# Kernel optimization log

Measured on AMD Instinct MI355X. Metric: run time of the kernel, lower is better.

## Reference

```python
import jax, jax.numpy as jnp
import numpy as np

R, N, C, E, H, NC = 25, 256, 64, 128, 8, 27


def _layernorm(x, w, b, axes, eps):
    m = x.mean(axis=axes, keepdims=True)
    v = x.var(axis=axes, keepdims=True)
    return (x - m) / jnp.sqrt(v + eps) * w + b


def _mha(emb_ln, idx, WQ, WK):
    # emb_ln: (R*N, E); idx: (L,) district indices
    ew = emb_ln.reshape(R, N, E)[idx]                       # (L,N,E) gather of district blocks
    Q = jnp.einsum('lne,hfe->lhnf', ew, WQ)                 # torch Linear: x @ W.T
    K = jnp.einsum('lne,hfe->lhnf', ew, WK)
    QK = jnp.einsum('lhnf,lhmf->lhnm', Q, K) / jnp.sqrt(jnp.float32(E))
    return jax.nn.softmax(QK, axis=2)                       # torch softmax(dim=1) over (L,n,n)


def setup_inputs() -> dict:
    key = jax.random.key(0)
    ks = jax.random.split(key, 16)
    inp = {
        'business_structure_target': jax.random.normal(ks[0], (R, C, N, 4), jnp.float32),
        'business_structure_infected': jax.random.normal(ks[1], (R, C, N, 4), jnp.float32),
        'customer_structure_target': jax.random.normal(ks[2], (R, C, N, NC, 4), jnp.float32),
        'customer_structure_infected': jax.random.normal(ks[3], (R, C, N, NC, 4), jnp.float32),
        'index_target_idx': jax.random.randint(ks[4], (R, C), 0, R),
        'index_infected_idx': jax.random.randint(ks[5], (R, C), 0, R),
        'covid_outbreak_business': jax.random.randint(ks[6], (R, C), 0, N),
        'emb_table': jax.random.normal(ks[7], (R * N, E), jnp.float32),
        'ln_emb_w': jnp.ones((E,), jnp.float32),
        'ln_emb_b': jnp.zeros((E,), jnp.float32),
        'WQ_trg': jax.random.normal(ks[8], (H, E, E), jnp.float32) * 0.05,
        'WK_trg': jax.random.normal(ks[9], (H, E, E), jnp.float32) * 0.05,
        'WQ_inf': jax.random.normal(ks[10], (H, E, E), jnp.float32) * 0.05,
        'WK_inf': jax.random.normal(ks[11], (H, E, E), jnp.float32) * 0.05,
        'W_os': jax.random.normal(ks[12], (E, E), jnp.float32) * 0.05,
        'b_os': jnp.zeros((E,), jnp.float32),
        'bs_w': jnp.ones((C, N), jnp.float32), 'bs_b': jnp.zeros((C, N), jnp.float32),
        'cs_w': jnp.ones((C, N), jnp.float32), 'cs_b': jnp.zeros((C, N), jnp.float32),
        'os_w': jnp.ones((C, N), jnp.float32), 'os_b': jnp.zeros((C, N), jnp.float32),
    }
    return inp


def reference(business_structure_target, business_structure_infected,
              customer_structure_target, customer_structure_infected,
              index_target_idx, index_infected_idx, covid_outbreak_business,
              emb_table, ln_emb_w, ln_emb_b,
              WQ_trg, WK_trg, WQ_inf, WK_inf,
              W_os, b_os, bs_w, bs_b, cs_w, cs_b, os_w, os_b):
    # mean over feature dim, then slicing per original forward
    bst = business_structure_target.mean(-1)[:R, 0]        # (R,N)
    bsi = business_structure_infected.mean(-1)[0]          # (C,N)
    cst = customer_structure_target.mean(-1)[:R, 0]        # (R,N,NC)
    csi = customer_structure_infected.mean(-1)[0]          # (C,N,NC)

    emb_ln = _layernorm(emb_table, ln_emb_w, ln_emb_b, -1, 1e-16)
    idx_t = index_target_idx[:R, 0]                        # (R,)
    idx_i = index_infected_idx[0]                          # (C,)

    attn_t = _mha(emb_ln, idx_t, WQ_trg, WK_trg)           # (R,H,N,N)
    BR_t = jnp.einsum('ln,lhnm->lmh', bst, attn_t)         # (R,N,H)
    attn_i = _mha(emb_ln, idx_i, WQ_inf, WK_inf)           # (C,H,N,N)
    BR_i = jnp.einsum('cn,chnm->cmh', bsi, attn_i)         # (C,N,H)

    # cosine similarity over head dim, broadcast (R,1,N,H) x (1,C,N,H)
    a = BR_t[:, None]
    b = BR_i[None]
    dot = jnp.sum(a * b, -1)
    na = jnp.linalg.norm(a, axis=-1)
    nb = jnp.linalg.norm(b, axis=-1)
    BS = dot / jnp.maximum(na * nb, 1e-15)                 # (R,C,N)

    # Jensen-Shannon-style KLD over consumer dim (log_target=True semantics)
    log_p = jax.nn.log_softmax(cst, -1)[:, None]           # (R,1,N,NC)
    log_q = jax.nn.log_softmax(csi, -1)[None]              # (1,C,N,NC)
    log_m = jax.nn.log_softmax((log_p + log_q) / 2, -1)
    kl_p = (jnp.exp(log_m) * (log_m - log_p)).mean(-1)
    kl_q = (jnp.exp(log_m) * (log_m - log_q)).mean(-1)
    CS = -(kl_p + kl_q) / 2                                # (R,C,N)

    biz = covid_outbreak_business[0]                       # (C,)
    inf_emb = emb_table[idx_i * N + biz]                   # (C,E) raw (non-LN) embedding
    proj = inf_emb @ W_os.T + b_os
    OS = (proj @ emb_table.T).reshape(C, R, N).transpose(1, 0, 2)  # (R,C,N)

    BS = _layernorm(BS, bs_w, bs_b, (-2, -1), 1e-5)
    CS = _layernorm(CS, cs_w, cs_b, (-2, -1), 1e-5)
    OS = _layernorm(OS, os_w, os_b, (-2, -1), 1e-5)
    return BS, CS, OS
```

## Files before the change

kernel.cpp:

```cpp
#include <hip/hip_runtime.h>
#include <math.h>

#define R_ 25
#define N_ 256
#define C_ 64
#define E_ 128
#define H_ 8
#define NC_ 27
#define SQS 28

typedef _Float16 f16x8 __attribute__((ext_vector_type(8)));
typedef float f32x16 __attribute__((ext_vector_type(16)));

union HU { ushort s; _Float16 h; };
__device__ __forceinline__ ushort ftoh(float f) { HU u; u.h = (_Float16)f; return u.s; }
__device__ __forceinline__ float htof(ushort s) { HU u; u.s = s; return (float)u.h; }

__device__ __forceinline__ float waveReduceSum(float v) {
  #pragma unroll
  for (int off = 32; off > 0; off >>= 1) v += __shfl_xor(v, off);
  return v;
}

__global__ __launch_bounds__(256) void k_prep(
    const float* __restrict__ emb, const float* __restrict__ ln_w,
    const float* __restrict__ ln_b, ushort* __restrict__ emb16,
    const float* __restrict__ bus_t, const float* __restrict__ bus_i,
    float* __restrict__ bst, float* __restrict__ bsi,
    const float* __restrict__ cus_t, const float* __restrict__ cus_i,
    float* __restrict__ Ssq, float* __restrict__ Tsq,
    const int* __restrict__ idx_t, const int* __restrict__ idx_i,
    int* __restrict__ cnt, int* __restrict__ lst,
    const int* __restrict__ biz, const float* __restrict__ Wos,
    const float* __restrict__ bos, float* __restrict__ projb) {
  __shared__ float er2[2][E_];
  int bid = blockIdx.x, t = threadIdx.x;
  if (bid < 1600) {
    int row = bid * 4 + (t >> 6);
    int lane = t & 63;
    const float2* x = (const float2*)(emb + (size_t)row * E_);
    float2 v = x[lane];
    float s = waveReduceSum(v.x + v.y);
    float m = s * (1.0f / 128.0f);
    float d0 = v.x - m, d1 = v.y - m;
    float ss = waveReduceSum(d0 * d0 + d1 * d1);
    float inv = 1.0f / sqrtf(ss * (1.0f / 128.0f) + 1e-16f);
    float2 wv = ((const float2*)ln_w)[lane];
    float2 bv = ((const float2*)ln_b)[lane];
    uint u = (uint)ftoh(d0 * inv * wv.x + bv.x) | ((uint)ftoh(d1 * inv * wv.y + bv.y) << 16);
    ((uint*)emb16)[(size_t)row * 64 + lane] = u;
  } else if (bid < 1689) {
    int i = (bid - 1600) * 256 + t;
    if (i < R_ * N_) {
      size_t row = (size_t)(i >> 8) * (C_ * N_) + (i & 255);
      float4 v = *(const float4*)&bus_t[row * 4];
      bst[i] = (v.x + v.y + v.z + v.w) * 0.25f;
    }
    int j = i - R_ * N_;
    if (j >= 0 && j < C_ * N_) {
      float4 v = *(const float4*)&bus_i[(size_t)j * 4];
      bsi[j] = (v.x + v.y + v.z + v.w) * 0.25f;
    }
  } else if (bid < 1778) {
    int i = (bid - 1689) * 256 + t;
    const float* src; float* dst; size_t base; int oi;
    if (i < R_ * N_) {
      src = cus_t; dst = Ssq; oi = i;
      base = ((size_t)(i >> 8) * (C_ * N_) + (i & 255)) * (NC_ * 4);
    } else {
      int j = i - R_ * N_;
      if (j >= C_ * N_) return;
      src = cus_i; dst = Tsq; oi = j;
      base = ((size_t)(j >> 8) * N_ + (j & 255)) * (NC_ * 4);
    }
    float v[NC_];
    float mx = -1e30f;
    #pragma unroll
    for (int j = 0; j < NC_; ++j) {
      float4 q = *(const float4*)&src[base + j * 4];
      v[j] = (q.x + q.y + q.z + q.w) * 0.25f;
      mx = fmaxf(mx, v[j]);
    }
    float se = 0.0f;
    #pragma unroll
    for (int j = 0; j < NC_; ++j) se += expf(v[j] - mx);
    float lse = mx + logf(se);
    #pragma unroll
    for (int j = 0; j < NC_; ++j) dst[(size_t)oi * SQS + j] = expf(0.5f * (v[j] - lse));
    dst[(size_t)oi * SQS + NC_] = 0.0f;
  } else if (bid == 1778) {
    if (t < 2 * R_) cnt[t] = 0;
    __syncthreads();
    if (t < R_) {
      int rr = idx_t[t * C_];
      int pos = atomicAdd(&cnt[rr], 1);
      lst[rr * 64 + pos] = t;
    }
    if (t < C_) {
      int rr = idx_i[t];
      int pos = atomicAdd(&cnt[R_ + rr], 1);
      lst[(R_ + rr) * 64 + pos] = t;
    }
  } else {
    int pb = bid - 1779;
    int ci = t >> 7, f = t & 127;
    int c = pb * 2 + ci;
    int row = idx_i[c] * N_ + biz[c];
    er2[ci][f] = emb[(size_t)row * E_ + f];
    __syncthreads();
    float acc = bos[f];
    const float* wr = &Wos[(size_t)f * E_];
    const float* er = er2[ci];
    for (int e = 0; e < E_; e += 4) {
      float4 w4 = *(const float4*)&wr[e];
      acc += er[e] * w4.x + er[e + 1] * w4.y + er[e + 2] * w4.z + er[e + 3] * w4.w;
    }
    projb[c * E_ + f] = acc;
  }
}

__global__ __launch_bounds__(512) void k_gt_mfma(
    const float* __restrict__ WQt_, const float* __restrict__ WKt_,
    const float* __restrict__ WQi_, const float* __restrict__ WKi_,
    ushort* __restrict__ Gt) {
  int h = blockIdx.x, set = blockIdx.y;
  const float* WQ = (set ? WQi_ : WQt_) + ((size_t)h << 14);
  const float* WK = (set ? WKi_ : WKt_) + ((size_t)h << 14);
  __shared__ uint QT[128 * 64];
  __shared__ uint KT[128 * 64];
  int t = threadIdx.x;
  for (int j = t; j < 8192; j += 512) {
    int e = j & 127, f2 = j >> 7;
    int wi = (f2 << 8) + e;
    float q0 = WQ[wi], q1 = WQ[wi + 128];
    float k0 = WK[wi], k1 = WK[wi + 128];
    int idx = (e << 6) + (f2 ^ ((e & 15) << 2));
    QT[idx] = (uint)ftoh(q0) | ((uint)ftoh(q1) << 16);
    KT[idx] = (uint)ftoh(k0) | ((uint)ftoh(k1) << 16);
  }
  __syncthreads();
  int w = t >> 6, l = t & 63, lo = l & 31, hi = l >> 5;
  int m0 = (w & 3) << 5, n0 = (w >> 2) << 6;
  f32x16 acc[2];
  #pragma unroll
  for (int i = 0; i < 2; ++i)
    #pragma unroll
    for (int j = 0; j < 16; ++j) acc[i][j] = 0.0f;
  int mrow = m0 + lo;
  #pragma unroll
  for (int ks = 0; ks < 8; ++ks) {
    int f2b = (ks << 3) + (hi << 2);
    f16x8 a = *(const f16x8*)&KT[(mrow << 6) + (f2b ^ ((mrow & 15) << 2))];
    #pragma unroll
    for (int tl = 0; tl < 2; ++tl) {
      int ncol = n0 + (tl << 5) + lo;
      f16x8 b = *(const f16x8*)&QT[(ncol << 6) + (f2b ^ ((ncol & 15) << 2))];
      acc[tl] = __builtin_amdgcn_mfma_f32_32x32x16_f16(a, b, acc[tl], 0, 0, 0);
    }
  }
  const float scale = 0.08838834764831845f;
  ushort* Go = Gt + (((size_t)(set * H_ + h)) << 14);
  #pragma unroll
  for (int tl = 0; tl < 2; ++tl)
    #pragma unroll
    for (int rg = 0; rg < 16; ++rg) {
      int row = m0 + (rg & 3) + ((rg >> 2) << 3) + (hi << 2);
      int col = n0 + (tl << 5) + lo;
      Go[(row << 7) + col] = ftoh(acc[tl][rg] * scale);
    }
}

__global__ __launch_bounds__(512) void k_attn_fused(
    const ushort* __restrict__ emb16, const ushort* __restrict__ GtAll,
    const int* __restrict__ cnt, const int* __restrict__ lst,
    const float* __restrict__ bst, const float* __restrict__ bsi,
    float* __restrict__ BRt, float* __restrict__ BRi) {
  int r = blockIdx.x, h = blockIdx.y, set = blockIdx.z;
  int g = set * R_ + r;
  int L = cnt[g];
  if (L == 0) return;
  __shared__ ushort ELN[256 * 128];
  __shared__ ushort TA[128 * 128];
  __shared__ ushort TB[128 * 128];
  __shared__ float redA[8 * 128];
  __shared__ float redB[8 * 128];
  __shared__ float gM[128], gD[128];
  int t = threadIdx.x;
  const uint4* Ep = (const uint4*)(emb16 + ((size_t)r << 15));
  for (int c = t; c < 4096; c += 512) {
    int n = c >> 4, s = c & 15;
    uint4 v = Ep[c];
    *(uint4*)&ELN[(n << 7) + ((s << 3) ^ ((n & 15) << 3))] = v;
  }
  const uint4* Gp = (const uint4*)(GtAll + ((size_t)(set * H_ + h) << 14));
  for (int c = t; c < 2048; c += 512) {
    int e2 = c >> 4, s = c & 15;
    uint4 v = Gp[c];
    *(uint4*)&TA[(e2 << 7) + ((s << 3) ^ ((e2 & 15) << 3))] = v;
  }
  __syncthreads();
  int w = t >> 6, l = t & 63, lo = l & 31, hi = l >> 5;
  f32x16 tacc[4];
  #pragma unroll
  for (int i = 0; i < 4; ++i)
    #pragma unroll
    for (int j = 0; j < 16; ++j) tacc[i][j] = 0.0f;
  int n = (w << 5) + lo;
  #pragma unroll
  for (int ks = 0; ks < 8; ++ks) {
    f16x8 a = *(const f16x8*)&ELN[(n << 7) + (((ks << 4) + (hi << 3)) ^ ((n & 15) << 3))];
    #pragma unroll
    for (int tl = 0; tl < 4; ++tl) {
      int f = (tl << 5) + lo;
      f16x8 b = *(const f16x8*)&TA[(f << 7) + (((ks << 4) + (hi << 3)) ^ ((f & 15) << 3))];
      tacc[tl] = __builtin_amdgcn_mfma_f32_32x32x16_f16(a, b, tacc[tl], 0, 0, 0);
    }
  }
  __syncthreads();
  {
    ushort* Tl = (w < 4) ? TA : TB;
    #pragma unroll
    for (int tl = 0; tl < 4; ++tl)
      #pragma unroll
      for (int rg = 0; rg < 16; ++rg) {
        int row = ((w & 3) << 5) + (rg & 3) + ((rg >> 2) << 3) + (hi << 2);
        int col = (tl << 5) + lo;
        Tl[(row << 7) + (col ^ ((row & 15) << 3))] = ftoh(tacc[tl][rg]);
      }
  }
  __syncthreads();
  const float* wv = set ? bsi : bst;
  float* BR = set ? BRi : BRt;
  const ushort* Tl = (w < 4) ? TA : TB;
  int rrow = n & 127;
  int baseRow = (w << 5) + (hi << 2);
  for (int mh = 0; mh < 2; ++mh) {
    f32x16 acc[4];
    #pragma unroll
    for (int i = 0; i < 4; ++i)
      #pragma unroll
      for (int j = 0; j < 16; ++j) acc[i][j] = 0.0f;
    #pragma unroll
    for (int ks = 0; ks < 8; ++ks) {
      f16x8 a = *(const f16x8*)&Tl[(rrow << 7) + (((ks << 4) + (hi << 3)) ^ ((rrow & 15) << 3))];
      #pragma unroll
      for (int tl = 0; tl < 4; ++tl) {
        int m = (mh << 7) + (tl << 5) + lo;
        f16x8 b = *(const f16x8*)&ELN[(m << 7) + (((ks << 4) + (hi << 3)) ^ ((m & 15) << 3))];
        acc[tl] = __builtin_amdgcn_mfma_f32_32x32x16_f16(a, b, acc[tl], 0, 0, 0);
      }
    }
    #pragma unroll
    for (int tl = 0; tl < 4; ++tl) {
      float mx = acc[tl][0];
      #pragma unroll
      for (int rg = 1; rg < 16; ++rg) mx = fmaxf(mx, acc[tl][rg]);
      mx = fmaxf(mx, __shfl_xor(mx, 32));
      if (hi == 0) redA[(w << 7) + (tl << 5) + lo] = mx;
    }
    __syncthreads();
    if (t < 128) {
      float gm = redA[t];
      #pragma unroll
      for (int ww = 1; ww < 8; ++ww) gm = fmaxf(gm, redA[(ww << 7) + t]);
      gM[t] = gm;
    }
    __syncthreads();
    #pragma unroll
    for (int tl = 0; tl < 4; ++tl) {
      float gmv = gM[(tl << 5) + lo];
      float s = 0.0f;
      #pragma unroll
      for (int rg = 0; rg < 16; ++rg) {
        acc[tl][rg] = __expf(acc[tl][rg] - gmv);
        s += acc[tl][rg];
      }
      s += __shfl_xor(s, 32);
      if (hi == 0) redB[(w << 7) + (tl << 5) + lo] = s;
    }
    __syncthreads();
    if (t < 128) {
      float d = 0.0f;
      #pragma unroll
      for (int ww = 0; ww < 8; ++ww) d += redB[(ww << 7) + t];
      gD[t] = d;
    }
    __syncthreads();
    for (int li = 0; li < L; ++li) {
      int ll = lst[g * 64 + li];
      float wreg[16];
      #pragma unroll
      for (int rg = 0; rg < 16; ++rg)
        wreg[rg] = wv[ll * N_ + baseRow + (rg & 3) + ((rg >> 2) << 3)];
      #pragma unroll
      for (int tl = 0; tl < 4; ++tl) {
        float part = 0.0f;
        #pragma unroll
        for (int rg = 0; rg < 16; ++rg) part += wreg[rg] * acc[tl][rg];
        part += __shfl_xor(part, 32);
        if (hi == 0) redA[(w << 7) + (tl << 5) + lo] = part;
      }
      __syncthreads();
      if (t < 128) {
        float s = 0.0f;
        #pragma unroll
        for (int ww = 0; ww < 8; ++ww) s += redA[(ww << 7) + t];
        BR[((size_t)ll * N_ + (mh << 7) + t) * H_ + h] = s / gD[t];
      }
      __syncthreads();
    }
  }
}

__global__ __launch_bounds__(256) void k_bscs_os(
    const float* __restrict__ BRt, const float* __restrict__ BRi,
    const float* __restrict__ Ssq, const float* __restrict__ Tsq,
    const float* __restrict__ emb, const float* __restrict__ projb,
    float* __restrict__ outBS, float* __restrict__ outCS,
    float* __restrict__ outOS) {
  __shared__ float pr[8][E_];
  int bid = blockIdx.x, t = threadIdx.x;
  if (bid < 1600) {
    int i = bid * 256 + t;
    int n = i & 255, c = (i >> 8) & 63, l = i >> 14;
    const float4* a = (const float4*)&BRt[((size_t)l * N_ + n) * H_];
    const float4* b = (const float4*)&BRi[((size_t)c * N_ + n) * H_];
    float4 a0 = a[0], a1 = a[1], b0 = b[0], b1 = b[1];
    float dot = a0.x * b0.x + a0.y * b0.y + a0.z * b0.z + a0.w * b0.w
              + a1.x * b1.x + a1.y * b1.y + a1.z * b1.z + a1.w * b1.w;
    float na = a0.x * a0.x + a0.y * a0.y + a0.z * a0.z + a0.w * a0.w
             + a1.x * a1.x + a1.y * a1.y + a1.z * a1.z + a1.w * a1.w;
    float nb = b0.x * b0.x + b0.y * b0.y + b0.z * b0.z + b0.w * b0.w
             + b1.x * b1.x + b1.y * b1.y + b1.z * b1.z + b1.w * b1.w;
    outBS[i] = dot / fmaxf(sqrtf(na) * sqrtf(nb), 1e-15f);

    const float4* sp = (const float4*)&Ssq[((size_t)l * N_ + n) * SQS];
    const float4* tp = (const float4*)&Tsq[((size_t)c * N_ + n) * SQS];
    float d2 = 0.0f;
    #pragma unroll
    for (int j = 0; j < 7; ++j) {
      float4 sv = sp[j], tv = tp[j];
      d2 += sv.x * tv.x + sv.y * tv.y + sv.z * tv.z + sv.w * tv.w;
    }
    outCS[i] = logf(d2) * (1.0f / 27.0f);
  } else {
    int o = bid - 1600;
    int l = o >> 3, cg = o & 7;
    for (int i = t; i < 1024; i += 256)
      pr[i >> 7][i & 127] = projb[(cg * 8 + (i >> 7)) * E_ + (i & 127)];
    __syncthreads();
    const float* er = &emb[((size_t)(l * N_) + t) << 7];
    float acc[8] = {0, 0, 0, 0, 0, 0, 0, 0};
    for (int e = 0; e < 128; e += 4) {
      float4 v = *(const float4*)&er[e];
      #pragma unroll
      for (int c = 0; c < 8; ++c)
        acc[c] += v.x * pr[c][e] + v.y * pr[c][e + 1] + v.z * pr[c][e + 2] + v.w * pr[c][e + 3];
    }
    #pragma unroll
    for (int c = 0; c < 8; ++c)
      outOS[((size_t)l * C_ + cg * 8 + c) * N_ + t] = acc[c];
  }
}

__global__ __launch_bounds__(1024) void k_ln_final(float* __restrict__ out,
    const float* __restrict__ w0, const float* __restrict__ b0,
    const float* __restrict__ w1, const float* __restrict__ b1,
    const float* __restrict__ w2, const float* __restrict__ b2) {
  int r = blockIdx.x, o = blockIdx.y;
  const float* w = (o == 0) ? w0 : ((o == 1) ? w1 : w2);
  const float* b = (o == 0) ? b0 : ((o == 1) ? b1 : b2);
  float* x = out + (size_t)o * 409600 + (size_t)r * 16384;
  int t = threadIdx.x;
  __shared__ float redm[16];
  float s = 0.0f;
  for (int i = t; i < 16384; i += 1024) s += x[i];
  s = waveReduceSum(s);
  if ((t & 63) == 0) redm[t >> 6] = s;
  __syncthreads();
  float m = 0.0f;
  #pragma unroll
  for (int k = 0; k < 16; ++k) m += redm[k];
  m *= (1.0f / 16384.0f);
  __syncthreads();
  float ss = 0.0f;
  for (int i = t; i < 16384; i += 1024) { float d = x[i] - m; ss += d * d; }
  ss = waveReduceSum(ss);
  if ((t & 63) == 0) redm[t >> 6] = ss;
  __syncthreads();
  float v = 0.0f;
  #pragma unroll
  for (int k = 0; k < 16; ++k) v += redm[k];
  v *= (1.0f / 16384.0f);
  float inv = 1.0f / sqrtf(v + 1e-5f);
  for (int i = t; i < 16384; i += 1024) x[i] = (x[i] - m) * inv * w[i] + b[i];
}

extern "C" void kernel_launch(void* const* d_in, const int* in_sizes, int n_in,
                              void* d_out, int out_size, void* d_ws, size_t ws_size,
                              hipStream_t stream) {
  const float* bus_t  = (const float*)d_in[0];
  const float* bus_i  = (const float*)d_in[1];
  const float* cus_t  = (const float*)d_in[2];
  const float* cus_i  = (const float*)d_in[3];
  const int*   idx_t  = (const int*)d_in[4];
  const int*   idx_i  = (const int*)d_in[5];
  const int*   cov    = (const int*)d_in[6];
  const float* emb    = (const float*)d_in[7];
  const float* ln_w   = (const float*)d_in[8];
  const float* ln_b   = (const float*)d_in[9];
  const float* WQ_trg = (const float*)d_in[10];
  const float* WK_trg = (const float*)d_in[11];
  const float* WQ_inf = (const float*)d_in[12];
  const float* WK_inf = (const float*)d_in[13];
  const float* W_os   = (const float*)d_in[14];
  const float* b_os   = (const float*)d_in[15];
  const float* bs_w   = (const float*)d_in[16];
  const float* bs_b   = (const float*)d_in[17];
  const float* cs_w   = (const float*)d_in[18];
  const float* cs_b   = (const float*)d_in[19];
  const float* os_w   = (const float*)d_in[20];
  const float* os_b   = (const float*)d_in[21];

  float* ws = (float*)d_ws;
  ushort* emb16 = (ushort*)ws;
  float* p = ws + 409600;
  ushort* Gt = (ushort*)p;   p += 131072;
  float* bst = p;            p += 6400;
  float* bsi = p;            p += 16384;
  float* Ssq = p;            p += R_ * N_ * SQS;
  float* Tsq = p;            p += C_ * N_ * SQS;
  float* BRt = p;            p += 51200;
  float* BRi = p;            p += 131072;
  float* projb = p;          p += 8192;
  int* cnt = (int*)p;        p += 64;
  int* lst = (int*)p;        p += 3200;

  float* outBS = (float*)d_out;
  float* outCS = outBS + 409600;
  float* outOS = outCS + 409600;

  k_prep<<<1811, 256, 0, stream>>>(emb, ln_w, ln_b, emb16,
                                   bus_t, bus_i, bst, bsi,
                                   cus_t, cus_i, Ssq, Tsq,
                                   idx_t, idx_i, cnt, lst,
                                   cov, W_os, b_os, projb);
  k_gt_mfma<<<dim3(H_, 2), 512, 0, stream>>>(WQ_trg, WK_trg, WQ_inf, WK_inf, Gt);
  k_attn_fused<<<dim3(R_, H_, 2), 512, 0, stream>>>(emb16, Gt, cnt, lst,
                                                    bst, bsi, BRt, BRi);
  k_bscs_os<<<1800, 256, 0, stream>>>(BRt, BRi, Ssq, Tsq, emb, projb,
                                      outBS, outCS, outOS);
  k_ln_final<<<dim3(R_, 3), 1024, 0, stream>>>(outBS, bs_w, bs_b, cs_w, cs_b, os_w, os_b);
}
```

Before: 84.19 us.

## Fuse all stages into one persistent kernel with software grid barriers

Replaces the five kernel launches with a single persistent kernel of 256 blocks that loops over work units and separates phases with atomic-counter grid barriers. Each attention unit now recomputes the per-head Gram matrix and the layer-normed fp16 embedding block locally, which removes the emb16/Gt intermediates and the gather lists. The final layernorm switches to a one-pass sum/sum-of-squares. This saves launch gaps and intermediate traffic but duplicates the Gram and layernorm work across districts, and it relies on all 256 blocks being co-resident for the spin barrier. The one-pass variance is also less numerically robust.

```diff
diff --git a/kernel.cpp b/kernel.cpp
--- a/kernel.cpp
+++ b/kernel.cpp
@@ -8,6 +8,7 @@
 #define H_ 8
 #define NC_ 27
 #define SQS 28
+#define NBLK 256
 
 typedef _Float16 f16x8 __attribute__((ext_vector_type(8)));
 typedef float f32x16 __attribute__((ext_vector_type(16)));
@@ -22,309 +23,323 @@
   return v;
 }
 
-__global__ __launch_bounds__(256) void k_prep(
-    const float* __restrict__ emb, const float* __restrict__ ln_w,
-    const float* __restrict__ ln_b, ushort* __restrict__ emb16,
-    const float* __restrict__ bus_t, const float* __restrict__ bus_i,
-    float* __restrict__ bst, float* __restrict__ bsi,
-    const float* __restrict__ cus_t, const float* __restrict__ cus_i,
-    float* __restrict__ Ssq, float* __restrict__ Tsq,
-    const int* __restrict__ idx_t, const int* __restrict__ idx_i,
-    int* __restrict__ cnt, int* __restrict__ lst,
-    const int* __restrict__ biz, const float* __restrict__ Wos,
-    const float* __restrict__ bos, float* __restrict__ projb) {
-  __shared__ float er2[2][E_];
-  int bid = blockIdx.x, t = threadIdx.x;
-  if (bid < 1600) {
-    int row = bid * 4 + (t >> 6);
-    int lane = t & 63;
-    const float2* x = (const float2*)(emb + (size_t)row * E_);
-    float2 v = x[lane];
-    float s = waveReduceSum(v.x + v.y);
-    float m = s * (1.0f / 128.0f);
-    float d0 = v.x - m, d1 = v.y - m;
-    float ss = waveReduceSum(d0 * d0 + d1 * d1);
-    float inv = 1.0f / sqrtf(ss * (1.0f / 128.0f) + 1e-16f);
-    float2 wv = ((const float2*)ln_w)[lane];
-    float2 bv = ((const float2*)ln_b)[lane];
-    uint u = (uint)ftoh(d0 * inv * wv.x + bv.x) | ((uint)ftoh(d1 * inv * wv.y + bv.y) << 16);
-    ((uint*)emb16)[(size_t)row * 64 + lane] = u;
-  } else if (bid < 1689) {
-    int i = (bid - 1600) * 256 + t;
-    if (i < R_ * N_) {
-      size_t row = (size_t)(i >> 8) * (C_ * N_) + (i & 255);
-      float4 v = *(const float4*)&bus_t[row * 4];
-      bst[i] = (v.x + v.y + v.z + v.w) * 0.25f;
-    }
-    int j = i - R_ * N_;
-    if (j >= 0 && j < C_ * N_) {
-      float4 v = *(const float4*)&bus_i[(size_t)j * 4];
-      bsi[j] = (v.x + v.y + v.z + v.w) * 0.25f;
-    }
-  } else if (bid < 1778) {
-    int i = (bid - 1689) * 256 + t;
-    const float* src; float* dst; size_t base; int oi;
-    if (i < R_ * N_) {
-      src = cus_t; dst = Ssq; oi = i;
-      base = ((size_t)(i >> 8) * (C_ * N_) + (i & 255)) * (NC_ * 4);
+__device__ __forceinline__ void gbar(int* cnt, int* flag) {
+  __syncthreads();
+  if (threadIdx.x == 0) {
+    __threadfence();
+    int prev = atomicAdd(cnt, 1);
+    if (prev == (int)gridDim.x - 1) {
+      atomicExch(flag, 1);
     } else {
-      int j = i - R_ * N_;
-      if (j >= C_ * N_) return;
-      src = cus_i; dst = Tsq; oi = j;
-      base = ((size_t)(j >> 8) * N_ + (j & 255)) * (NC_ * 4);
-    }
-    float v[NC_];
-    float mx = -1e30f;
-    #pragma unroll
-    for (int j = 0; j < NC_; ++j) {
-      float4 q = *(const float4*)&src[base + j * 4];
-      v[j] = (q.x + q.y + q.z + q.w) * 0.25f;
-      mx = fmaxf(mx, v[j]);
-    }
-    float se = 0.0f;
-    #pragma unroll
-    for (int j = 0; j < NC_; ++j) se += expf(v[j] - mx);
-    float lse = mx + logf(se);
-    #pragma unroll
-    for (int j = 0; j < NC_; ++j) dst[(size_t)oi * SQS + j] = expf(0.5f * (v[j] - lse));
-    dst[(size_t)oi * SQS + NC_] = 0.0f;
-  } else if (bid == 1778) {
-    if (t < 2 * R_) cnt[t] = 0;
-    __syncthreads();
-    if (t < R_) {
-      int rr = idx_t[t * C_];
-      int pos = atomicAdd(&cnt[rr], 1);
-      lst[rr * 64 + pos] = t;
-    }
-    if (t < C_) {
-      int rr = idx_i[t];
-      int pos = atomicAdd(&cnt[R_ + rr], 1);
-      lst[(R_ + rr) * 64 + pos] = t;
-    }
-  } else {
-    int pb = bid - 1779;
-    int ci = t >> 7, f = t & 127;
-    int c = pb * 2 + ci;
-    int row = idx_i[c] * N_ + biz[c];
-    er2[ci][f] = emb[(size_t)row * E_ + f];
-    __syncthreads();
-    float acc = bos[f];
-    const float* wr = &Wos[(size_t)f * E_];
-    const float* er = er2[ci];
-    for (int e = 0; e < E_; e += 4) {
-      float4 w4 = *(const float4*)&wr[e];
-      acc += er[e] * w4.x + er[e + 1] * w4.y + er[e + 2] * w4.z + er[e + 3] * w4.w;
-    }
-    projb[c * E_ + f] = acc;
-  }
-}
-
-__global__ __launch_bounds__(512) void k_gt_mfma(
-    const float* __restrict__ WQt_, const float* __restrict__ WKt_,
-    const float* __restrict__ WQi_, const float* __restrict__ WKi_,
-    ushort* __restrict__ Gt) {
-  int h = blockIdx.x, set = blockIdx.y;
-  const float* WQ = (set ? WQi_ : WQt_) + ((size_t)h << 14);
-  const float* WK = (set ? WKi_ : WKt_) + ((size_t)h << 14);
-  __shared__ uint QT[128 * 64];
-  __shared__ uint KT[128 * 64];
-  int t = threadIdx.x;
-  for (int j = t; j < 8192; j += 512) {
-    int e = j & 127, f2 = j >> 7;
-    int wi = (f2 << 8) + e;
-    float q0 = WQ[wi], q1 = WQ[wi + 128];
-    float k0 = WK[wi], k1 = WK[wi + 128];
-    int idx = (e << 6) + (f2 ^ ((e & 15) << 2));
-    QT[idx] = (uint)ftoh(q0) | ((uint)ftoh(q1) << 16);
-    KT[idx] = (uint)ftoh(k0) | ((uint)ftoh(k1) << 16);
+      while (atomicAdd(flag, 0) == 0) { __builtin_amdgcn_s_sleep(2); }
+    }
+    __threadfence();
   }
   __syncthreads();
+}
+
+__global__ __launch_bounds__(512) void k_mega(
+    const float* __restrict__ bus_t, const float* __restrict__ bus_i,
+    const float* __restrict__ cus_t, const float* __restrict__ cus_i,
+    const int* __restrict__ idx_t, const int* __restrict__ idx_i,
+    const int* __restrict__ cov,
+    const float* __restrict__ emb, const float* __restrict__ ln_w,
+    const float* __restrict__ ln_b,
+    const float* __restrict__ WQt, const float* __restrict__ WKt,
+    const float* __restrict__ WQi, const float* __restrict__ WKi,
+    const float* __restrict__ Wos, const float* __restrict__ bos,
+    const float* __restrict__ bs_w, const float* __restrict__ bs_b,
+    const float* __restrict__ cs_w, const float* __restrict__ cs_b,
+    const float* __restrict__ os_w, const float* __restrict__ os_b,
+    float* __restrict__ Ssq, float* __restrict__ Tsq,
+    float* __restrict__ BRt, float* __restrict__ BRi,
+    float* __restrict__ outBS, float* __restrict__ outCS,
+    float* __restrict__ outOS, int* __restrict__ bar) {
+  __shared__ uint smemU[35200];
+  ushort* ELN = (ushort*)smemU;
+  ushort* TA  = (ushort*)(smemU + 16384);
+  ushort* TB  = (ushort*)(smemU + 24576);
+  float* redA = (float*)(smemU + 32768);
+  float* redB = (float*)(smemU + 33792);
+  float* gM   = (float*)(smemU + 34816);
+  float* gD   = (float*)(smemU + 34944);
+  int* llist  = (int*)(smemU + 35072);
+  int* lcnt   = (int*)(smemU + 35136);
+  int t = threadIdx.x;
   int w = t >> 6, l = t & 63, lo = l & 31, hi = l >> 5;
-  int m0 = (w & 3) << 5, n0 = (w >> 2) << 6;
-  f32x16 acc[2];
-  #pragma unroll
-  for (int i = 0; i < 2; ++i)
-    #pragma unroll
-    for (int j = 0; j < 16; ++j) acc[i][j] = 0.0f;
-  int mrow = m0 + lo;
-  #pragma unroll
-  for (int ks = 0; ks < 8; ++ks) {
-    int f2b = (ks << 3) + (hi << 2);
-    f16x8 a = *(const f16x8*)&KT[(mrow << 6) + (f2b ^ ((mrow & 15) << 2))];
-    #pragma unroll
-    for (int tl = 0; tl < 2; ++tl) {
-      int ncol = n0 + (tl << 5) + lo;
-      f16x8 b = *(const f16x8*)&QT[(ncol << 6) + (f2b ^ ((ncol & 15) << 2))];
-      acc[tl] = __builtin_amdgcn_mfma_f32_32x32x16_f16(a, b, acc[tl], 0, 0, 0);
+  const float scale = 0.08838834764831845f;
+
+  for (int u = blockIdx.x; u < 678; u += NBLK) {
+    if (u < 400) {
+      int r = u % 25, hh = (u / 25) & 7, set = u / 200;
+      if (t == 0) *lcnt = 0;
+      __syncthreads();
+      if (set == 0) { if (t < R_ && idx_t[t * C_] == r) llist[atomicAdd(lcnt, 1)] = t; }
+      else          { if (t < C_ && idx_i[t] == r)      llist[atomicAdd(lcnt, 1)] = t; }
+      __syncthreads();
+      int L = *lcnt;
+      if (L == 0) continue;
+      const float* WQ = (set ? WQi : WQt) + ((size_t)hh << 14);
+      const float* WK = (set ? WKi : WKt) + ((size_t)hh << 14);
+      uint* QT = (uint*)TA; uint* KT = (uint*)TB;
+      for (int j = t; j < 8192; j += 512) {
+        int e = j & 127, f2 = j >> 7;
+        int wi = (f2 << 8) + e;
+        uint qp = (uint)ftoh(WQ[wi]) | ((uint)ftoh(WQ[wi + 128]) << 16);
+        uint kp = (uint)ftoh(WK[wi]) | ((uint)ftoh(WK[wi + 128]) << 16);
+        int idx = (e << 6) + (f2 ^ ((e & 15) << 2));
+        QT[idx] = qp; KT[idx] = kp;
+      }
+      for (int pass = 0; pass < 32; ++pass) {
+        int row = pass * 8 + w;
+        const float2* x = (const float2*)(emb + ((size_t)(r * N_ + row) << 7));
+        float2 v = x[l];
+        float s = waveReduceSum(v.x + v.y);
+        float m = s * (1.0f / 128.0f);
+        float d0 = v.x - m, d1 = v.y - m;
+        float ss = waveReduceSum(d0 * d0 + d1 * d1);
+        float inv = 1.0f / sqrtf(ss * (1.0f / 128.0f) + 1e-16f);
+        float2 wv2 = ((const float2*)ln_w)[l];
+        float2 bv2 = ((const float2*)ln_b)[l];
+        uint pk = (uint)ftoh(d0 * inv * wv2.x + bv2.x) |
+                  ((uint)ftoh(d1 * inv * wv2.y + bv2.y) << 16);
+        ((uint*)ELN)[((row << 7) + ((l << 1) ^ ((row & 15) << 3))) >> 1] = pk;
+      }
+      __syncthreads();
+      f32x16 gacc[2];
+      #pragma unroll
+      for (int i = 0; i < 2; ++i)
+        #pragma unroll
+        for (int j = 0; j < 16; ++j) gacc[i][j] = 0.0f;
+      {
+        int mrow = ((w & 3) << 5) + lo;
+        #pragma unroll
+        for (int ks = 0; ks < 8; ++ks) {
+          int f2b = (ks << 3) + (hi << 2);
+          f16x8 a = *(const f16x8*)&KT[(mrow << 6) + (f2b ^ ((mrow & 15) << 2))];
+          #pragma unroll
+          for (int tl = 0; tl < 2; ++tl) {
+            int ncol = ((w >> 2) << 6) + (tl << 5) + lo;
+            f16x8 b = *(const f16x8*)&QT[(ncol << 6) + (f2b ^ ((ncol & 15) << 2))];
+            gacc[tl] = __builtin_amdgcn_mfma_f32_32x32x16_f16(a, b, gacc[tl], 0, 0, 0);
+          }
+        }
+      }
+      __syncthreads();
+      #pragma unroll
+      for (int tl = 0; tl < 2; ++tl)
+        #pragma unroll
+        for (int rg = 0; rg < 16; ++rg) {
+          int row = ((w & 3) << 5) + (rg & 3) + ((rg >> 2) << 3) + (hi << 2);
+          int col = ((w >> 2) << 6) + (tl << 5) + lo;
+          TA[(row << 7) + (col ^ ((row & 15) << 3))] = ftoh(gacc[tl][rg] * scale);
+        }
+      __syncthreads();
+      f32x16 tacc[4];
+      #pragma unroll
+      for (int i = 0; i < 4; ++i)
+        #pragma unroll
+        for (int j = 0; j < 16; ++j) tacc[i][j] = 0.0f;
+      int n = (w << 5) + lo;
+      #pragma unroll
+      for (int ks = 0; ks < 8; ++ks) {
+        f16x8 a = *(const f16x8*)&ELN[(n << 7) + (((ks << 4) + (hi << 3)) ^ ((n & 15) << 3))];
+        #pragma unroll
+        for (int tl = 0; tl < 4; ++tl) {
+          int f = (tl << 5) + lo;
+          f16x8 b = *(const f16x8*)&TA[(f << 7) + (((ks << 4) + (hi << 3)) ^ ((f & 15) << 3))];
+          tacc[tl] = __builtin_amdgcn_mfma_f32_32x32x16_f16(a, b, tacc[tl], 0, 0, 0);
+        }
+      }
+      __syncthreads();
+      {
+        ushort* Tl = (w < 4) ? TA : TB;
+        #pragma unroll
+        for (int tl = 0; tl < 4; ++tl)
+          #pragma unroll
+          for (int rg = 0; rg < 16; ++rg) {
+            int row = ((w & 3) << 5) + (rg & 3) + ((rg >> 2) << 3) + (hi << 2);
+            int col = (tl << 5) + lo;
+            Tl[(row << 7) + (col ^ ((row & 15) << 3))] = ftoh(tacc[tl][rg]);
+          }
+      }
+      __syncthreads();
+      const float* busp = set ? bus_i : bus_t;
+      size_t lstride = set ? (size_t)N_ : (size_t)C_ * N_;
+      float* BR = set ? BRi : BRt;
+      const ushort* Tl = (w < 4) ? TA : TB;
+      int rrow = n & 127;
+      int baseRow = (w << 5) + (hi << 2);
+      for (int mh = 0; mh < 2; ++mh) {
+        f32x16 acc[4];
+        #pragma unroll
+        for (int i = 0; i < 4; ++i)
+          #pragma unroll
+          for (int j = 0; j < 16; ++j) acc[i][j] = 0.0f;
+        #pragma unroll
+        for (int ks = 0; ks < 8; ++ks) {
+          f16x8 a = *(const f16x8*)&Tl[(rrow << 7) + (((ks << 4) + (hi << 3)) ^ ((rrow & 15) << 3))];
+          #pragma unroll
+          for (int tl = 0; tl < 4; ++tl) {
+            int m = (mh << 7) + (tl << 5) + lo;
+            f16x8 b = *(const f16x8*)&ELN[(m << 7) + (((ks << 4) + (hi << 3)) ^ ((m & 15) << 3))];
+            acc[tl] = __builtin_amdgcn_mfma_f32_32x32x16_f16(a, b, acc[tl], 0, 0, 0);
+          }
+        }
+        #pragma unroll
+        for (int tl = 0; tl < 4; ++tl) {
+          float mx = acc[tl][0];
+          #pragma unroll
+          for (int rg = 1; rg < 16; ++rg) mx = fmaxf(mx, acc[tl][rg]);
+          mx = fmaxf(mx, __shfl_xor(mx, 32));
+          if (hi == 0) redA[(w << 7) + (tl << 5) + lo] = mx;
+        }
+        __syncthreads();
+        if (t < 128) {
+          float gm = redA[t];
+          #pragma unroll
+          for (int ww = 1; ww < 8; ++ww) gm = fmaxf(gm, redA[(ww << 7) + t]);
+          gM[t] = gm;
+        }
+        __syncthreads();
+        #pragma unroll
+        for (int tl = 0; tl < 4; ++tl) {
+          float gmv = gM[(tl << 5) + lo];
+          float s = 0.0f;
+          #pragma unroll
+          for (int rg = 0; rg < 16; ++rg) {
+            acc[tl][rg] = __expf(acc[tl][rg] - gmv);
+            s += acc[tl][rg];
+          }
+          s += __shfl_xor(s, 32);
+          if (hi == 0) redB[(w << 7) + (tl << 5) + lo] = s;
+        }
+        __syncthreads();
+        if (t < 128) {
+          float d = 0.0f;
+          #pragma unroll
+          for (int ww = 0; ww < 8; ++ww) d += redB[(ww << 7) + t];
+          gD[t] = d;
+        }
+        __syncthreads();
+        for (int li = 0; li < L; ++li) {
+          int ll = llist[li];
+          const float* wbase = busp + (lstride * ll + baseRow) * 4;
+          float wreg[16];
+          #pragma unroll
+          for (int rg = 0; rg < 16; ++rg) {
+            float4 v4 = *(const float4*)&wbase[(((rg >> 2) << 3) + (rg & 3)) * 4];
+            wreg[rg] = (v4.x + v4.y + v4.z + v4.w) * 0.25f;
+          }
+          #pragma unroll
+          for (int tl = 0; tl < 4; ++tl) {
+            float part = 0.0f;
+            #pragma unroll
+            for (int rg = 0; rg < 16; ++rg) part += wreg[rg] * acc[tl][rg];
+            part += __shfl_xor(part, 32);
+            if (hi == 0) redA[(w << 7) + (tl << 5) + lo] = part;
+          }
+          __syncthreads();
+          if (t < 128) {
+            float s = 0.0f;
+            #pragma unroll
+            for (int ww = 0; ww < 8; ++ww) s += redA[(ww << 7) + t];
+            BR[((size_t)ll * N_ + (mh << 7) + t) * H_ + hh] = s / gD[t];
+          }
+          __syncthreads();
+        }
+      }
+    } else if (u < 578) {
+      int gidx = (u - 400) * 512 + t;
+      int rowi = gidx >> 2, sub = gidx & 3;
+      const float* src; float* dst; size_t base; int oi;
+      if (rowi < R_ * N_) {
+        src = cus_t; dst = Ssq; oi = rowi;
+        base = ((size_t)(rowi >> 8) * (C_ * N_) + (rowi & 255)) * (NC_ * 4);
+      } else {
+        int j = rowi - R_ * N_;
+        src = cus_i; dst = Tsq; oi = j;
+        base = ((size_t)(j >> 8) * N_ + (j & 255)) * (NC_ * 4);
+      }
+      int j0 = sub * 7;
+      int nj = (sub == 3) ? 6 : 7;
+      float v[7];
+      float mx = -1e30f;
+      #pragma unroll
+      for (int k = 0; k < 7; ++k) {
+        if (k < nj) {
+          float4 q = *(const float4*)&src[base + (j0 + k) * 4];
+          v[k] = (q.x + q.y + q.z + q.w) * 0.25f;
+          mx = fmaxf(mx, v[k]);
+        }
+      }
+      mx = fmaxf(mx, __shfl_xor(mx, 1));
+      mx = fmaxf(mx, __shfl_xor(mx, 2));
+      float se = 0.0f;
+      #pragma unroll
+      for (int k = 0; k < 7; ++k) if (k < nj) se += expf(v[k] - mx);
+      se += __shfl_xor(se, 1);
+      se += __shfl_xor(se, 2);
+      float lse = mx + logf(se);
+      #pragma unroll
+      for (int k = 0; k < 7; ++k)
+        if (k < nj) dst[(size_t)oi * SQS + j0 + k] = expf(0.5f * (v[k] - lse));
+      if (sub == 3) dst[(size_t)oi * SQS + NC_] = 0.0f;
+    } else {
+      int v = u - 578;
+      int ll = v >> 2, c0 = (v & 3) * 16;
+      float* er16 = (float*)smemU;
+      float* pr16 = (float*)(smemU + 2048);
+      __syncthreads();
+      for (int j = t; j < 2048; j += 512) {
+        int ci = j >> 7, e = j & 127;
+        int row = idx_i[c0 + ci] * N_ + cov[c0 + ci];
+        er16[j] = emb[((size_t)row << 7) + e];
+      }
+      __syncthreads();
+      {
+        int id0 = t << 2;
+        int ci = id0 >> 7;
+        const float* er = &er16[ci << 7];
+        #pragma unroll
+        for (int k = 0; k < 4; ++k) {
+          int f = (id0 & 127) + k;
+          const float* wr = &Wos[(size_t)f << 7];
+          float acc = bos[f];
+          for (int e = 0; e < 128; e += 4) {
+            float4 w4 = *(const float4*)&wr[e];
+            acc += er[e] * w4.x + er[e + 1] * w4.y + er[e + 2] * w4.z + er[e + 3] * w4.w;
+          }
+          pr16[(ci << 7) + (id0 & 127) + k] = acc;
+        }
+      }
+      __syncthreads();
+      {
+        int nn = t & 255, ch = t >> 8;
+        const float* er = emb + ((size_t)(ll * N_ + nn) << 7);
+        float acc[8] = {0, 0, 0, 0, 0, 0, 0, 0};
+        for (int e = 0; e < 128; e += 4) {
+          float4 v4 = *(const float4*)&er[e];
+          #pragma unroll
+          for (int j = 0; j < 8; ++j) {
+            const float* pj = &pr16[((ch * 8 + j) << 7) + e];
+            acc[j] += v4.x * pj[0] + v4.y * pj[1] + v4.z * pj[2] + v4.w * pj[3];
+          }
+        }
+        #pragma unroll
+        for (int j = 0; j < 8; ++j)
+          outOS[((size_t)ll * C_ + c0 + ch * 8 + j) * N_ + nn] = acc[j];
+      }
+      __syncthreads();
     }
   }
-  const float scale = 0.08838834764831845f;
-  ushort* Go = Gt + (((size_t)(set * H_ + h)) << 14);
-  #pragma unroll
-  for (int tl = 0; tl < 2; ++tl)
-    #pragma unroll
-    for (int rg = 0; rg < 16; ++rg) {
-      int row = m0 + (rg & 3) + ((rg >> 2) << 3) + (hi << 2);
-      int col = n0 + (tl << 5) + lo;
-      Go[(row << 7) + col] = ftoh(acc[tl][rg] * scale);
-    }
-}
-
-__global__ __launch_bounds__(512) void k_attn_fused(
-    const ushort* __restrict__ emb16, const ushort* __restrict__ GtAll,
-    const int* __restrict__ cnt, const int* __restrict__ lst,
-    const float* __restrict__ bst, const float* __restrict__ bsi,
-    float* __restrict__ BRt, float* __restrict__ BRi) {
-  int r = blockIdx.x, h = blockIdx.y, set = blockIdx.z;
-  int g = set * R_ + r;
-  int L = cnt[g];
-  if (L == 0) return;
-  __shared__ ushort ELN[256 * 128];
-  __shared__ ushort TA[128 * 128];
-  __shared__ ushort TB[128 * 128];
-  __shared__ float redA[8 * 128];
-  __shared__ float redB[8 * 128];
-  __shared__ float gM[128], gD[128];
-  int t = threadIdx.x;
-  const uint4* Ep = (const uint4*)(emb16 + ((size_t)r << 15));
-  for (int c = t; c < 4096; c += 512) {
-    int n = c >> 4, s = c & 15;
-    uint4 v = Ep[c];
-    *(uint4*)&ELN[(n << 7) + ((s << 3) ^ ((n & 15) << 3))] = v;
-  }
-  const uint4* Gp = (const uint4*)(GtAll + ((size_t)(set * H_ + h) << 14));
-  for (int c = t; c < 2048; c += 512) {
-    int e2 = c >> 4, s = c & 15;
-    uint4 v = Gp[c];
-    *(uint4*)&TA[(e2 << 7) + ((s << 3) ^ ((e2 & 15) << 3))] = v;
-  }
-  __syncthreads();
-  int w = t >> 6, l = t & 63, lo = l & 31, hi = l >> 5;
-  f32x16 tacc[4];
-  #pragma unroll
-  for (int i = 0; i < 4; ++i)
-    #pragma unroll
-    for (int j = 0; j < 16; ++j) tacc[i][j] = 0.0f;
-  int n = (w << 5) + lo;
-  #pragma unroll
-  for (int ks = 0; ks < 8; ++ks) {
-    f16x8 a = *(const f16x8*)&ELN[(n << 7) + (((ks << 4) + (hi << 3)) ^ ((n & 15) << 3))];
-    #pragma unroll
-    for (int tl = 0; tl < 4; ++tl) {
-      int f = (tl << 5) + lo;
-      f16x8 b = *(const f16x8*)&TA[(f << 7) + (((ks << 4) + (hi << 3)) ^ ((f & 15) << 3))];
-      tacc[tl] = __builtin_amdgcn_mfma_f32_32x32x16_f16(a, b, tacc[tl], 0, 0, 0);
-    }
-  }
-  __syncthreads();
-  {
-    ushort* Tl = (w < 4) ? TA : TB;
-    #pragma unroll
-    for (int tl = 0; tl < 4; ++tl)
-      #pragma unroll
-      for (int rg = 0; rg < 16; ++rg) {
-        int row = ((w & 3) << 5) + (rg & 3) + ((rg >> 2) << 3) + (hi << 2);
-        int col = (tl << 5) + lo;
-        Tl[(row << 7) + (col ^ ((row & 15) << 3))] = ftoh(tacc[tl][rg]);
-      }
-  }
-  __syncthreads();
-  const float* wv = set ? bsi : bst;
-  float* BR = set ? BRi : BRt;
-  const ushort* Tl = (w < 4) ? TA : TB;
-  int rrow = n & 127;
-  int baseRow = (w << 5) + (hi << 2);
-  for (int mh = 0; mh < 2; ++mh) {
-    f32x16 acc[4];
-    #pragma unroll
-    for (int i = 0; i < 4; ++i)
-      #pragma unroll
-      for (int j = 0; j < 16; ++j) acc[i][j] = 0.0f;
-    #pragma unroll
-    for (int ks = 0; ks < 8; ++ks) {
-      f16x8 a = *(const f16x8*)&Tl[(rrow << 7) + (((ks << 4) + (hi << 3)) ^ ((rrow & 15) << 3))];
-      #pragma unroll
-      for (int tl = 0; tl < 4; ++tl) {
-        int m = (mh << 7) + (tl << 5) + lo;
-        f16x8 b = *(const f16x8*)&ELN[(m << 7) + (((ks << 4) + (hi << 3)) ^ ((m & 15) << 3))];
-        acc[tl] = __builtin_amdgcn_mfma_f32_32x32x16_f16(a, b, acc[tl], 0, 0, 0);
-      }
-    }
-    #pragma unroll
-    for (int tl = 0; tl < 4; ++tl) {
-      float mx = acc[tl][0];
-      #pragma unroll
-      for (int rg = 1; rg < 16; ++rg) mx = fmaxf(mx, acc[tl][rg]);
-      mx = fmaxf(mx, __shfl_xor(mx, 32));
-      if (hi == 0) redA[(w << 7) + (tl << 5) + lo] = mx;
-    }
-    __syncthreads();
-    if (t < 128) {
-      float gm = redA[t];
-      #pragma unroll
-      for (int ww = 1; ww < 8; ++ww) gm = fmaxf(gm, redA[(ww << 7) + t]);
-      gM[t] = gm;
-    }
-    __syncthreads();
-    #pragma unroll
-    for (int tl = 0; tl < 4; ++tl) {
-      float gmv = gM[(tl << 5) + lo];
-      float s = 0.0f;
-      #pragma unroll
-      for (int rg = 0; rg < 16; ++rg) {
-        acc[tl][rg] = __expf(acc[tl][rg] - gmv);
-        s += acc[tl][rg];
-      }
-      s += __shfl_xor(s, 32);
-      if (hi == 0) redB[(w << 7) + (tl << 5) + lo] = s;
-    }
-    __syncthreads();
-    if (t < 128) {
-      float d = 0.0f;
-      #pragma unroll
-      for (int ww = 0; ww < 8; ++ww) d += redB[(ww << 7) + t];
-      gD[t] = d;
-    }
-    __syncthreads();
-    for (int li = 0; li < L; ++li) {
-      int ll = lst[g * 64 + li];
-      float wreg[16];
-      #pragma unroll
-      for (int rg = 0; rg < 16; ++rg)
-        wreg[rg] = wv[ll * N_ + baseRow + (rg & 3) + ((rg >> 2) << 3)];
-      #pragma unroll
-      for (int tl = 0; tl < 4; ++tl) {
-        float part = 0.0f;
-        #pragma unroll
-        for (int rg = 0; rg < 16; ++rg) part += wreg[rg] * acc[tl][rg];
-        part += __shfl_xor(part, 32);
-        if (hi == 0) redA[(w << 7) + (tl << 5) + lo] = part;
-      }
-      __syncthreads();
-      if (t < 128) {
-        float s = 0.0f;
-        #pragma unroll
-        for (int ww = 0; ww < 8; ++ww) s += redA[(ww << 7) + t];
-        BR[((size_t)ll * N_ + (mh << 7) + t) * H_ + h] = s / gD[t];
-      }
-      __syncthreads();
-    }
-  }
-}
-
-__global__ __launch_bounds__(256) void k_bscs_os(
-    const float* __restrict__ BRt, const float* __restrict__ BRi,
-    const float* __restrict__ Ssq, const float* __restrict__ Tsq,
-    const float* __restrict__ emb, const float* __restrict__ projb,
-    float* __restrict__ outBS, float* __restrict__ outCS,
-    float* __restrict__ outOS) {
-  __shared__ float pr[8][E_];
-  int bid = blockIdx.x, t = threadIdx.x;
-  if (bid < 1600) {
-    int i = bid * 256 + t;
-    int n = i & 255, c = (i >> 8) & 63, l = i >> 14;
-    const float4* a = (const float4*)&BRt[((size_t)l * N_ + n) * H_];
-    const float4* b = (const float4*)&BRi[((size_t)c * N_ + n) * H_];
+  gbar(&bar[0], &bar[1]);
+
+  for (int u = blockIdx.x; u < 800; u += NBLK) {
+    int i = u * 512 + t;
+    int nn = i & 255, c = (i >> 8) & 63, ll = i >> 14;
+    const float4* a = (const float4*)&BRt[((size_t)ll * N_ + nn) * H_];
+    const float4* b = (const float4*)&BRi[((size_t)c * N_ + nn) * H_];
     float4 a0 = a[0], a1 = a[1], b0 = b[0], b1 = b[1];
     float dot = a0.x * b0.x + a0.y * b0.y + a0.z * b0.z + a0.w * b0.w
               + a1.x * b1.x + a1.y * b1.y + a1.z * b1.z + a1.w * b1.w;
@@ -333,9 +348,8 @@
     float nb = b0.x * b0.x + b0.y * b0.y + b0.z * b0.z + b0.w * b0.w
              + b1.x * b1.x + b1.y * b1.y + b1.z * b1.z + b1.w * b1.w;
     outBS[i] = dot / fmaxf(sqrtf(na) * sqrtf(nb), 1e-15f);
-
-    const float4* sp = (const float4*)&Ssq[((size_t)l * N_ + n) * SQS];
-    const float4* tp = (const float4*)&Tsq[((size_t)c * N_ + n) * SQS];
+    const float4* sp = (const float4*)&Ssq[((size_t)ll * N_ + nn) * SQS];
+    const float4* tp = (const float4*)&Tsq[((size_t)c * N_ + nn) * SQS];
     float d2 = 0.0f;
     #pragma unroll
     for (int j = 0; j < 7; ++j) {
@@ -343,57 +357,41 @@
       d2 += sv.x * tv.x + sv.y * tv.y + sv.z * tv.z + sv.w * tv.w;
     }
     outCS[i] = logf(d2) * (1.0f / 27.0f);
-  } else {
-    int o = bid - 1600;
-    int l = o >> 3, cg = o & 7;
-    for (int i = t; i < 1024; i += 256)
-      pr[i >> 7][i & 127] = projb[(cg * 8 + (i >> 7)) * E_ + (i & 127)];
+  }
+  gbar(&bar[2], &bar[3]);
+
+  for (int u = blockIdx.x; u < 75; u += NBLK) {
+    int r = u / 3, o = u % 3;
+    float* x = (o == 0) ? outBS : (o == 1) ? outCS : outOS;
+    x += (size_t)r * 16384;
+    const float* wv = (o == 0) ? bs_w : (o == 1) ? cs_w : os_w;
+    const float* bv = (o == 0) ? bs_b : (o == 1) ? cs_b : os_b;
+    float s = 0.0f, q = 0.0f;
+    for (int k = 0; k < 32; ++k) {
+      float v = x[k * 512 + t];
+      s += v; q += v * v;
+    }
+    s = waveReduceSum(s);
+    q = waveReduceSum(q);
+    if (l == 0) { redA[w * 2] = s; redA[w * 2 + 1] = q; }
     __syncthreads();
-    const float* er = &emb[((size_t)(l * N_) + t) << 7];
-    float acc[8] = {0, 0, 0, 0, 0, 0, 0, 0};
-    for (int e = 0; e < 128; e += 4) {
-      float4 v = *(const float4*)&er[e];
-      #pragma unroll
-      for (int c = 0; c < 8; ++c)
-        acc[c] += v.x * pr[c][e] + v.y * pr[c][e + 1] + v.z * pr[c][e + 2] + v.w * pr[c][e + 3];
-    }
-    #pragma unroll
-    for (int c = 0; c < 8; ++c)
-      outOS[((size_t)l * C_ + cg * 8 + c) * N_ + t] = acc[c];
+    if (t == 0) {
+      float S = 0, Q = 0;
+      #pragma unroll
+      for (int k = 0; k < 8; ++k) { S += redA[k * 2]; Q += redA[k * 2 + 1]; }
+      float m = S * (1.0f / 16384.0f);
+      float var = Q * (1.0f / 16384.0f) - m * m;
+      redB[0] = m;
+      redB[1] = 1.0f / sqrtf(var + 1e-5f);
+    }
+    __syncthreads();
+    float m = redB[0], inv = redB[1];
+    for (int k = 0; k < 32; ++k) {
+      int pos = k * 512 + t;
+      x[pos] = (x[pos] - m) * inv * wv[pos] + bv[pos];
+    }
+    __syncthreads();
   }
-}
-
-__global__ __launch_bounds__(1024) void k_ln_final(float* __restrict__ out,
-    const float* __restrict__ w0, const float* __restrict__ b0,
-    const float* __restrict__ w1, const float* __restrict__ b1,
-    const float* __restrict__ w2, const float* __restrict__ b2) {
-  int r = blockIdx.x, o = blockIdx.y;
-  const float* w = (o == 0) ? w0 : ((o == 1) ? w1 : w2);
-  const float* b = (o == 0) ? b0 : ((o == 1) ? b1 : b2);
-  float* x = out + (size_t)o * 409600 + (size_t)r * 16384;
-  int t = threadIdx.x;
-  __shared__ float redm[16];
-  float s = 0.0f;
-  for (int i = t; i < 16384; i += 1024) s += x[i];
-  s = waveReduceSum(s);
-  if ((t & 63) == 0) redm[t >> 6] = s;
-  __syncthreads();
-  float m = 0.0f;
-  #pragma unroll
-  for (int k = 0; k < 16; ++k) m += redm[k];
-  m *= (1.0f / 16384.0f);
-  __syncthreads();
-  float ss = 0.0f;
-  for (int i = t; i < 16384; i += 1024) { float d = x[i] - m; ss += d * d; }
-  ss = waveReduceSum(ss);
-  if ((t & 63) == 0) redm[t >> 6] = ss;
-  __syncthreads();
-  float v = 0.0f;
-  #pragma unroll
-  for (int k = 0; k < 16; ++k) v += redm[k];
-  v *= (1.0f / 16384.0f);
-  float inv = 1.0f / sqrtf(v + 1e-5f);
-  for (int i = t; i < 16384; i += 1024) x[i] = (x[i] - m) * inv * w[i] + b[i];
 }
 
 extern "C" void kernel_launch(void* const* d_in, const int* in_sizes, int n_in,
@@ -422,33 +420,24 @@
   const float* os_w   = (const float*)d_in[20];
   const float* os_b   = (const float*)d_in[21];
 
-  float* ws = (float*)d_ws;
-  ushort* emb16 = (ushort*)ws;
-  float* p = ws + 409600;
-  ushort* Gt = (ushort*)p;   p += 131072;
-  float* bst = p;            p += 6400;
-  float* bsi = p;            p += 16384;
+  float* p = (float*)d_ws;
   float* Ssq = p;            p += R_ * N_ * SQS;
   float* Tsq = p;            p += C_ * N_ * SQS;
   float* BRt = p;            p += 51200;
   float* BRi = p;            p += 131072;
-  float* projb = p;          p += 8192;
-  int* cnt = (int*)p;        p += 64;
-  int* lst = (int*)p;        p += 3200;
+  int* bar = (int*)p;        p += 8;
 
   float* outBS = (float*)d_out;
   float* outCS = outBS + 409600;
   float* outOS = outCS + 409600;
 
-  k_prep<<<1811, 256, 0, stream>>>(emb, ln_w, ln_b, emb16,
-                                   bus_t, bus_i, bst, bsi,
-                                   cus_t, cus_i, Ssq, Tsq,
-                                   idx_t, idx_i, cnt, lst,
-                                   cov, W_os, b_os, projb);
-  k_gt_mfma<<<dim3(H_, 2), 512, 0, stream>>>(WQ_trg, WK_trg, WQ_inf, WK_inf, Gt);
-  k_attn_fused<<<dim3(R_, H_, 2), 512, 0, stream>>>(emb16, Gt, cnt, lst,
-                                                    bst, bsi, BRt, BRi);
-  k_bscs_os<<<1800, 256, 0, stream>>>(BRt, BRi, Ssq, Tsq, emb, projb,
-                                      outBS, outCS, outOS);
-  k_ln_final<<<dim3(R_, 3), 1024, 0, stream>>>(outBS, bs_w, bs_b, cs_w, cs_b, os_w, os_b);
+  hipMemsetAsync(bar, 0, 8 * sizeof(int), stream);
+  k_mega<<<NBLK, 512, 0, stream>>>(bus_t, bus_i, cus_t, cus_i,
+                                   idx_t, idx_i, cov,
+                                   emb, ln_w, ln_b,
+                                   WQ_trg, WK_trg, WQ_inf, WK_inf,
+                                   W_os, b_os,
+                                   bs_w, bs_b, cs_w, cs_b, os_w, os_b,
+                                   Ssq, Tsq, BRt, BRi,
+                                   outBS, outCS, outOS, bar);
 }
```

Measured after the change: 212.5 us. 152% more time.
